# Performance work log

Measured on AMD Instinct MI355X. Metric: run time of the kernel, lower is better.

Reference implementation:

```python
import jax, jax.numpy as jnp
import numpy as np

B, S, D, H, DFF = 2, 2048, 768, 12, 3072
DK = D // H
LN_EPS = 1e-5

def _row_norm(x):
    # L2-normalize along last dim (torch F.normalize semantics)
    n = jnp.sqrt(jnp.sum(x * x, axis=-1, keepdims=True))
    return x / jnp.maximum(n, 1e-12)

def _layer_norm(x, gamma, beta):
    mu = jnp.mean(x, axis=-1, keepdims=True)
    var = jnp.mean((x - mu) ** 2, axis=-1, keepdims=True)
    return (x - mu) * jax.lax.rsqrt(var + LN_EPS) * gamma + beta

def setup_inputs() -> dict:
    key = jax.random.key(0)
    ks = jax.random.split(key, 16)
    sd = 1.0 / np.sqrt(D)
    sf = 1.0 / np.sqrt(DFF)
    inp = {
        "x": jax.random.normal(ks[0], (B, S, D), jnp.float32),
        "Wq": jax.random.uniform(ks[1], (D, D), jnp.float32, -sd, sd),
        "bq": jnp.zeros((D,), jnp.float32),
        "Wk": jax.random.uniform(ks[2], (D, D), jnp.float32, -sd, sd),
        "bk": jnp.zeros((D,), jnp.float32),
        "Wv": jax.random.uniform(ks[3], (D, D), jnp.float32, -sd, sd),
        "bv": jnp.zeros((D,), jnp.float32),
        "Wo": jax.random.uniform(ks[4], (D, D), jnp.float32, -sd, sd),
        "bo": jnp.zeros((D,), jnp.float32),
        "W1": jax.random.uniform(ks[5], (D, DFF), jnp.float32, -sd, sd),
        "b1": jnp.zeros((DFF,), jnp.float32),
        "W2": jax.random.uniform(ks[6], (DFF, D), jnp.float32, -sf, sf),
        "b2": jnp.zeros((D,), jnp.float32),
        "gamma": jnp.ones((D,), jnp.float32),
        "beta": jnp.zeros((D,), jnp.float32),
    }
    return inp

def reference(x, Wq, bq, Wk, bk, Wv, bv, Wo, bo, W1, b1, W2, b2, gamma, beta):
    b, s = x.shape[0], x.shape[1]
    # QKV projections, split into heads: [B,H,S,DK]
    def heads(y):
        return y.reshape(b, s, H, DK).transpose(0, 2, 1, 3)
    Q = heads(x @ Wq + bq)
    K = heads(x @ Wk + bk)
    V = heads(x @ Wv + bv)
    Qn = _row_norm(Q)
    Kn = _row_norm(K)
    scores = jnp.einsum("bhqd,bhkd->bhqk", Qn, Kn)
    attn = scores * scores  # squared dot-product, no softmax
    out = jnp.einsum("bhqk,bhkd->bhqd", attn, V)
    out = out.transpose(0, 2, 1, 3).reshape(b, s, D)
    attn_out = out @ Wo + bo
    x = _layer_norm(x + attn_out, gamma, beta)
    # FFN with exact GELU
    h = jax.nn.gelu(x @ W1 + b1, approximate=False)
    ff = h @ W2 + b2
    x = _layer_norm(x + ff, gamma, beta)  # norm1 reused
    return x
```

## Files before the change

### kernel.cpp

```cpp
#include <hip/hip_runtime.h>
#include <math.h>

using bf16   = __bf16;
using bf16x8 = __attribute__((ext_vector_type(8))) __bf16;
using bf16x4 = __attribute__((ext_vector_type(4))) __bf16;
using f32x4  = __attribute__((ext_vector_type(4))) float;

constexpr int S_   = 2048;
constexpr int D_   = 768;
constexpr int DFF_ = 3072;
constexpr int M_   = 4096;
constexpr int BH_  = 24;

__device__ __forceinline__ f32x4 mfma16(bf16x8 a, bf16x8 b, f32x4 c) {
    return __builtin_amdgcn_mfma_f32_16x16x32_bf16(a, b, c, 0, 0, 0);
}

__device__ __forceinline__ void gload16(const bf16* g, bf16* l) {
    __builtin_amdgcn_global_load_lds(
        (const __attribute__((address_space(1))) void*)g,
        (__attribute__((address_space(3))) void*)l, 16, 0, 0);
}

template<int N> __device__ __forceinline__ void wait_vmcnt() {
    if constexpr (N == 0)      asm volatile("s_waitcnt vmcnt(0)" ::: "memory");
    else if constexpr (N == 4) asm volatile("s_waitcnt vmcnt(4)" ::: "memory");
    else if constexpr (N == 6) asm volatile("s_waitcnt vmcnt(6)" ::: "memory");
    else if constexpr (N == 8) asm volatile("s_waitcnt vmcnt(8)" ::: "memory");
    else static_assert(N == 0, "unsupported vmcnt");
}
__device__ __forceinline__ void wait_lgkm0() {
    asm volatile("s_waitcnt lgkmcnt(0)" ::: "memory");
}

__device__ __forceinline__ int xcd_swz(int orig, int nwg) {
    return (orig & 7) * (nwg >> 3) + (orig >> 3);
}

__device__ __forceinline__ float gelu_f(float v) {
    float y = 1.5957691f * (v + 0.044715f * v * v * v);
    return v / (1.0f + __expf(-y));
}

__global__ __launch_bounds__(256)
void pack_x_kernel(const float* __restrict__ x, bf16* __restrict__ xb) {
    const int i = blockIdx.x * 256 + threadIdx.x;
    float4 v = ((const float4*)x)[i];
    bf16x4 o;
    o[0] = (bf16)v.x; o[1] = (bf16)v.y; o[2] = (bf16)v.z; o[3] = (bf16)v.w;
    ((bf16x4*)xb)[i] = o;
}

__global__ __launch_bounds__(256)
void merge_ao_kernel(const bf16* __restrict__ a, const bf16* __restrict__ b,
                     bf16* __restrict__ o) {
    const long i = ((long)blockIdx.x * 256 + threadIdx.x) * 8;
    bf16x8 va = *(const bf16x8*)&a[i];
    bf16x8 vb = *(const bf16x8*)&b[i];
    bf16x8 vo;
#pragma unroll
    for (int j = 0; j < 8; j++) vo[j] = (bf16)((float)va[j] + (float)vb[j]);
    *(bf16x8*)&o[i] = vo;
}

template<bool FIRST>
__global__ __launch_bounds__(256)
void merge_ln_kernel(const bf16* __restrict__ pp, const float* __restrict__ bias,
                     const float* __restrict__ residf, const bf16* __restrict__ residb,
                     const float* __restrict__ gamma, const float* __restrict__ beta,
                     float* __restrict__ outf, bf16* __restrict__ outb) {
    __shared__ float sa[4], sb[4];
    const int row = blockIdx.x, t = threadIdx.x;
    const bf16* p0 = pp + (long)row * 768;
    const bf16* p1 = pp + (long)M_ * 768 + (long)row * 768;
    float v[3];
#pragma unroll
    for (int i = 0; i < 3; i++) {
        const int c = t + i * 256;
        float y = (float)p0[c] + (float)p1[c] + bias[c];
        if (FIRST) y += residf[(long)row * 768 + c];
        else       y += (float)residb[(long)row * 768 + c];
        v[i] = y;
    }
    float s  = v[0] + v[1] + v[2];
    float ss = v[0] * v[0] + v[1] * v[1] + v[2] * v[2];
#pragma unroll
    for (int o = 32; o; o >>= 1) { s += __shfl_xor(s, o); ss += __shfl_xor(ss, o); }
    if ((t & 63) == 0) { sa[t >> 6] = s; sb[t >> 6] = ss; }
    __syncthreads();
    s  = sa[0] + sa[1] + sa[2] + sa[3];
    ss = sb[0] + sb[1] + sb[2] + sb[3];
    const float mu   = s * (1.0f / 768.0f);
    const float var  = ss * (1.0f / 768.0f) - mu * mu;
    const float rstd = rsqrtf(var + 1e-5f);
#pragma unroll
    for (int i = 0; i < 3; i++) {
        const int c = t + i * 256;
        const float ov = (v[i] - mu) * rstd * gamma[c] + beta[c];
        if (FIRST) outb[(long)row * 768 + c] = (bf16)ov;
        else       outf[(long)row * 768 + c] = ov;
    }
}

__global__ __launch_bounds__(256)
void wt_all_kernel(const float* __restrict__ Wq, const float* __restrict__ Wk,
                   const float* __restrict__ Wv, const float* __restrict__ Wo,
                   const float* __restrict__ W1, const float* __restrict__ W2,
                   bf16* __restrict__ Wqkvt, bf16* __restrict__ Wot,
                   bf16* __restrict__ W1t, bf16* __restrict__ W2t) {
    int bid = blockIdx.x;
    const float* in; bf16* out; int K, N, t;
    if (bid < 576) {
        int m = bid / 144; t = bid % 144; K = 768; N = 768;
        in  = (m == 0) ? Wq : (m == 1) ? Wk : (m == 2) ? Wv : Wo;
        out = (m == 3) ? Wot : Wqkvt + (size_t)m * 768 * 768;
    } else if (bid < 1152) {
        t = bid - 576; K = 768; N = 3072; in = W1; out = W1t;
    } else {
        t = bid - 1152; K = 3072; N = 768; in = W2; out = W2t;
    }
    const int ntx = N / 64;
    const int n0 = (t % ntx) * 64, k0 = (t / ntx) * 64;

    __shared__ __align__(16) bf16 T[64][72];
    const int tt = threadIdx.x;
    const int r  = tt >> 2, c0 = (tt & 3) * 16;
    const float* src = in + (size_t)(k0 + r) * N + n0 + c0;
#pragma unroll
    for (int j = 0; j < 16; j += 4) {
        float4 v = *(const float4*)(src + j);
        T[r][c0 + j + 0] = (bf16)v.x;
        T[r][c0 + j + 1] = (bf16)v.y;
        T[r][c0 + j + 2] = (bf16)v.z;
        T[r][c0 + j + 3] = (bf16)v.w;
    }
    __syncthreads();
    bf16x8 o0, o1;
#pragma unroll
    for (int j = 0; j < 8; j++) { o0[j] = T[c0 + j][r]; o1[j] = T[c0 + 8 + j][r]; }
    bf16* dst = out + (size_t)(n0 + r) * K + k0 + c0;
    *(bf16x8*)(dst)     = o0;
    *(bf16x8*)(dst + 8) = o1;
}

template<int EPI, int K, int BM, int BN, int WR, int WC, int KSPLIT>
__global__ __launch_bounds__(256)
void gemm_bt(const bf16* __restrict__ A, const bf16* __restrict__ Bt,
             const float* __restrict__ bias0, const float* __restrict__ bias1,
             const float* __restrict__ bias2,
             bf16* __restrict__ outb,
             bf16* __restrict__ qo, bf16* __restrict__ ko, bf16* __restrict__ vo) {
    constexpr int MR  = BM / WR / 16;
    constexpr int NR  = BN / WC / 16;
    constexpr int GA  = BM / 32;
    constexpr int GB  = BN / 32;
    constexpr int NPT = GA + GB;
    constexpr int KS  = K / KSPLIT;
    constexpr int NCOL = (EPI == 0) ? 2304 : (EPI == 2) ? 3072 : 768;
    constexpr int NBX  = NCOL / BN;
    __shared__ __align__(16) bf16 Al[2 * BM * 64];
    __shared__ __align__(16) bf16 Bl[2 * BN * 64];
    const int tid  = threadIdx.x;
    const int lane = tid & 63, w = tid >> 6;
    const int wr = w / WC, wc = w % WC;
    const int wg = xcd_swz(blockIdx.x, gridDim.x);
    const int ks = wg % KSPLIT;
    const int tt = wg / KSPLIT;
    const int m0 = (tt / NBX) * BM, n0 = (tt % NBX) * BN;
    const int kb = ks * KS;
    const int g = lane >> 4, q = lane & 15;
    const int srow = lane >> 3;
    const int schunk = (((lane & 7) ^ ((lane >> 3) & 7))) * 8;

    f32x4 acc[MR][NR] = {};

    const bf16* gaA = A  + (long)(m0 + w * (BM / 4) + srow) * K + kb + schunk;
    const bf16* gaB = Bt + (long)(n0 + w * (BN / 4) + srow) * K + kb + schunk;

    auto stage = [&](int buf, int kt) {
#pragma unroll
        for (int i = 0; i < GA; i++)
            gload16(gaA + kt + (long)i * 8 * K,
                    &Al[buf * BM * 64 + (w * (BM / 4) + i * 8) * 64]);
#pragma unroll
        for (int i = 0; i < GB; i++)
            gload16(gaB + kt + (long)i * 8 * K,
                    &Bl[buf * BN * 64 + (w * (BN / 4) + i * 8) * 64]);
    };
    auto compute = [&](int buf) {
#pragma unroll
        for (int c = 0; c < 2; c++) {
            const int rch = ((c * 4 + g) ^ (q & 7)) * 8;
            bf16x8 af[MR], bfr[NR];
#pragma unroll
            for (int i = 0; i < MR; i++)
                af[i] = *(const bf16x8*)
                    &Al[buf * BM * 64 + (wr * (BM / WR) + i * 16 + q) * 64 + rch];
#pragma unroll
            for (int i = 0; i < NR; i++)
                bfr[i] = *(const bf16x8*)
                    &Bl[buf * BN * 64 + (wc * (BN / WC) + i * 16 + q) * 64 + rch];
#pragma unroll
            for (int mi = 0; mi < MR; mi++)
#pragma unroll
                for (int ni = 0; ni < NR; ni++)
                    acc[mi][ni] = mfma16(af[mi], bfr[ni], acc[mi][ni]);
        }
    };

    stage(0, 0);
    stage(1, 64);
    int cur = 0;
    for (int kt = 0; kt < KS - 64; kt += 64) {
        wait_vmcnt<NPT>();
        __builtin_amdgcn_s_barrier();
        compute(cur);
        wait_lgkm0();
        __builtin_amdgcn_s_barrier();
        if (kt + 128 < KS) stage(cur, kt + 128);
        cur ^= 1;
    }
    wait_vmcnt<0>();
    __builtin_amdgcn_s_barrier();
    compute(cur);

#pragma unroll
    for (int mi = 0; mi < MR; mi++) {
        if (EPI == 0) {
            const int col0  = n0 + wc * 64;
            const int which = (col0 >= 1536) ? 2 : (col0 >= 768 ? 1 : 0);
            const int row0  = m0 + wr * (BM / WR) + mi * 16 + g * 4;
            float val[NR][4];
#pragma unroll
            for (int ni = 0; ni < NR; ni++) {
                const int dd = col0 + ni * 16 + q - which * 768;
                const float bias = (which == 0 ? bias0 : which == 1 ? bias1 : bias2)[dd];
#pragma unroll
                for (int r = 0; r < 4; r++) val[ni][r] = acc[mi][ni][r] + bias;
            }
            if (which <= 1) {
#pragma unroll
                for (int r = 0; r < 4; r++) {
                    float ss = val[0][r] * val[0][r];
#pragma unroll
                    for (int ni = 1; ni < NR; ni++) ss += val[ni][r] * val[ni][r];
                    ss += __shfl_xor(ss, 1);
                    ss += __shfl_xor(ss, 2);
                    ss += __shfl_xor(ss, 4);
                    ss += __shfl_xor(ss, 8);
                    const float rn = 1.0f / fmaxf(sqrtf(ss), 1e-12f);
#pragma unroll
                    for (int ni = 0; ni < NR; ni++) val[ni][r] *= rn;
                }
            }
            const int dd0 = col0 - which * 768;
            const int hh  = dd0 >> 6;
            const long bh = (long)(row0 >> 11) * 12 + hh;
#pragma unroll
            for (int ni = 0; ni < NR; ni++) {
                const int dk = ni * 16 + q;
                if (which == 2) {
                    bf16x4 pv;
#pragma unroll
                    for (int r = 0; r < 4; r++) pv[r] = (bf16)val[ni][r];
                    *(bf16x4*)&vo[(bh * 64 + dk) * 2048 + (row0 & 2047)] = pv;
                } else {
                    bf16* dst = (which == 0) ? qo : ko;
#pragma unroll
                    for (int r = 0; r < 4; r++)
                        dst[(bh * 2048 + ((row0 + r) & 2047)) * 64 + dk] = (bf16)val[ni][r];
                }
            }
        } else if (EPI == 2) {
#pragma unroll
            for (int ni = 0; ni < NR; ni++) {
                const int col  = n0 + wc * (BN / WC) + ni * 16 + q;
                const int row0 = m0 + wr * (BM / WR) + mi * 16 + g * 4;
                const float bias = bias0[col];
#pragma unroll
                for (int r = 0; r < 4; r++) {
                    const float v = acc[mi][ni][r] + bias;
                    outb[(long)(row0 + r) * 3072 + col] = (bf16)gelu_f(v);
                }
            }
        } else {
#pragma unroll
            for (int ni = 0; ni < NR; ni++) {
                const int col  = n0 + wc * (BN / WC) + ni * 16 + q;
                const int row0 = m0 + wr * (BM / WR) + mi * 16 + g * 4;
#pragma unroll
                for (int r = 0; r < 4; r++)
                    outb[(long)ks * M_ * 768 + (long)(row0 + r) * 768 + col] =
                        (bf16)acc[mi][ni][r];
            }
        }
    }
}

__global__ __launch_bounds__(256, 3)
void attn_kernel(const bf16* __restrict__ Qn, const bf16* __restrict__ Kn,
                 const bf16* __restrict__ Vt, bf16* __restrict__ AOp) {
    const int wg  = xcd_swz(blockIdx.x, gridDim.x);
    const int bh  = wg >> 5;
    const int rem = wg & 31;
    const int kvhalf = rem >> 4;
    const int qblk   = rem & 15;
    const int tid = threadIdx.x, lane = tid & 63, w = tid >> 6;
    const int g = lane >> 4, q15 = lane & 15;
    const int qbase = qblk * 128 + w * 32;
    const int kv0   = kvhalf * 1024;
    constexpr int NT = 16;

    __shared__ __align__(16) bf16 Kl[2][64][64];
    __shared__ __align__(16) bf16 Vl[2][64][64];
    __shared__ __align__(16) bf16 Pl[4][16][64];
    bf16 (*Pw)[64] = Pl[w];

    const bf16* Qp = Qn + (long)bh * S_ * 64;
    const bf16* Kp = Kn + (long)bh * S_ * 64 + (long)kv0 * 64;
    const bf16* Vp = Vt + (long)bh * 64 * S_ + kv0;
    bf16* AOo = AOp + (long)kvhalf * M_ * D_;

    const int srow = tid >> 3, scol = (tid & 7) * 8;
    const int ssw  = (((lane & 7) ^ ((lane >> 3) & 7))) * 8;
    const int q7   = q15 & 7;

    bf16x8 qf00 = *(const bf16x8*)&Qp[(long)(qbase + q15) * 64 + g * 8];
    bf16x8 qf01 = *(const bf16x8*)&Qp[(long)(qbase + q15) * 64 + 32 + g * 8];
    bf16x8 qf10 = *(const bf16x8*)&Qp[(long)(qbase + 16 + q15) * 64 + g * 8];
    bf16x8 qf11 = *(const bf16x8*)&Qp[(long)(qbase + 16 + q15) * 64 + 32 + g * 8];

    f32x4 o0[4] = {}, o1[4] = {};
    bf16x8 kf[4][2], vf[4][2];
    bf16x8 aK0, aK1, aV0, aV1, bK0, bK1, bV0, bV1;

    auto gloadA = [&](int kt) {
        aK0 = *(const bf16x8*)&Kp[(long)(kt + srow) * 64 + scol];
        aK1 = *(const bf16x8*)&Kp[(long)(kt + 32 + srow) * 64 + scol];
        aV0 = *(const bf16x8*)&Vp[(long)srow * S_ + kt + scol];
        aV1 = *(const bf16x8*)&Vp[(long)(32 + srow) * S_ + kt + scol];
    };
    auto gloadB = [&](int kt) {
        bK0 = *(const bf16x8*)&Kp[(long)(kt + srow) * 64 + scol];
        bK1 = *(const bf16x8*)&Kp[(long)(kt + 32 + srow) * 64 + scol];
        bV0 = *(const bf16x8*)&Vp[(long)srow * S_ + kt + scol];
        bV1 = *(const bf16x8*)&Vp[(long)(32 + srow) * S_ + kt + scol];
    };
    auto stageA = [&](int buf) {
        *(bf16x8*)&Kl[buf][srow][ssw]      = aK0;
        *(bf16x8*)&Kl[buf][32 + srow][ssw] = aK1;
        *(bf16x8*)&Vl[buf][srow][ssw]      = aV0;
        *(bf16x8*)&Vl[buf][32 + srow][ssw] = aV1;
    };
    auto stageB = [&](int buf) {
        *(bf16x8*)&Kl[buf][srow][ssw]      = bK0;
        *(bf16x8*)&Kl[buf][32 + srow][ssw] = bK1;
        *(bf16x8*)&Vl[buf][srow][ssw]      = bV0;
        *(bf16x8*)&Vl[buf][32 + srow][ssw] = bV1;
    };

    auto loadKf = [&](int cur) {
#pragma unroll
        for (int ni = 0; ni < 4; ni++)
#pragma unroll
            for (int c = 0; c < 2; c++)
                kf[ni][c] = *(const bf16x8*)
                    &Kl[cur][ni * 16 + q15][(((c * 4 + g) ^ q7)) * 8];
    };
    auto loadVf = [&](int cur) {
#pragma unroll
        for (int ni = 0; ni < 4; ni++)
#pragma unroll
            for (int c = 0; c < 2; c++)
                vf[ni][c] = *(const bf16x8*)
                    &Vl[cur][ni * 16 + q15][(((c * 4 + g) ^ q7)) * 8];
    };
    auto qk = [&](bf16x8 qa, bf16x8 qb) {
        f32x4 s[4];
#pragma unroll
        for (int ni = 0; ni < 4; ni++) {
            s[ni] = mfma16(kf[ni][0], qa, f32x4{0.f, 0.f, 0.f, 0.f});
            s[ni] = mfma16(kf[ni][1], qb, s[ni]);
        }
#pragma unroll
        for (int ni = 0; ni < 4; ni++) {
            bf16x4 p4;
#pragma unroll
            for (int r = 0; r < 4; r++) { float v = s[ni][r]; p4[r] = (bf16)(v * v); }
            const int ch = (ni * 2 + (g >> 1)) ^ q7;
            *(bf16x4*)&Pw[q15][ch * 8 + (g & 1) * 4] = p4;
        }
    };
    auto pv = [&](f32x4 (&o)[4]) {
        bf16x8 pf0 = *(const bf16x8*)&Pw[q15][((g ^ q7)) * 8];
        bf16x8 pf1 = *(const bf16x8*)&Pw[q15][(((4 + g) ^ q7)) * 8];
#pragma unroll
        for (int ni = 0; ni < 4; ni++) {
            o[ni] = mfma16(pf0, vf[ni][0], o[ni]);
            o[ni] = mfma16(pf1, vf[ni][1], o[ni]);
        }
    };

    gloadA(0);
    stageA(0);
    gloadB(64);
    wait_lgkm0(); __builtin_amdgcn_s_barrier();
    stageB(1);
    gloadA(2 * 64);
    loadKf(0); qk(qf00, qf01);
    loadVf(0); pv(o0);
    qk(qf10, qf11);

    for (int t = 1; t <= NT - 3; t += 2) {
        pv(o1);
        wait_lgkm0(); __builtin_amdgcn_s_barrier();
        stageA(0);
        gloadB((t + 2) * 64);
        loadKf(1); qk(qf00, qf01);
        loadVf(1); pv(o0);
        qk(qf10, qf11);

        pv(o1);
        wait_lgkm0(); __builtin_amdgcn_s_barrier();
        stageB(1);
        if (t + 3 < NT) gloadA((t + 3) * 64);
        loadKf(0); qk(qf00, qf01);
        loadVf(0); pv(o0);
        qk(qf10, qf11);
    }
    pv(o1);
    wait_lgkm0(); __builtin_amdgcn_s_barrier();
    loadKf(1); qk(qf00, qf01);
    loadVf(1); pv(o0);
    qk(qf10, qf11);
    pv(o1);

    const int b = bh / 12, h = bh % 12;
#pragma unroll
    for (int ni = 0; ni < 4; ni++)
#pragma unroll
        for (int r = 0; r < 4; r++) {
            const int s0r = qbase + g * 4 + r;
            AOo[((long)b * S_ + s0r) * D_ + h * 64 + ni * 16 + q15] = (bf16)o0[ni][r];
            const int s1r = qbase + 16 + g * 4 + r;
            AOo[((long)b * S_ + s1r) * D_ + h * 64 + ni * 16 + q15] = (bf16)o1[ni][r];
        }
}

extern "C" void kernel_launch(void* const* d_in, const int* in_sizes, int n_in,
                              void* d_out, int out_size, void* d_ws, size_t ws_size,
                              hipStream_t stream) {
    const float* x     = (const float*)d_in[0];
    const float* Wq    = (const float*)d_in[1];
    const float* bq    = (const float*)d_in[2];
    const float* Wk    = (const float*)d_in[3];
    const float* bk    = (const float*)d_in[4];
    const float* Wv    = (const float*)d_in[5];
    const float* bv    = (const float*)d_in[6];
    const float* Wo    = (const float*)d_in[7];
    const float* bo    = (const float*)d_in[8];
    const float* W1    = (const float*)d_in[9];
    const float* b1    = (const float*)d_in[10];
    const float* W2    = (const float*)d_in[11];
    const float* b2    = (const float*)d_in[12];
    const float* gamma = (const float*)d_in[13];
    const float* beta  = (const float*)d_in[14];

    char* p = (char*)d_ws;
    auto alloc = [&](size_t bytes) -> void* {
        void* r = p;
        p += (bytes + 255) & ~(size_t)255;
        return r;
    };
    bf16*  Xb    = (bf16*)alloc((size_t)M_ * D_ * 2);
    bf16*  Wqkvt = (bf16*)alloc((size_t)2304 * 768 * 2);
    bf16*  Wot   = (bf16*)alloc((size_t)768 * 768 * 2);
    bf16*  W1t   = (bf16*)alloc((size_t)3072 * 768 * 2);
    bf16*  W2t   = (bf16*)alloc((size_t)768 * 3072 * 2);
    bf16*  Qh    = (bf16*)alloc((size_t)BH_ * S_ * 64 * 2);
    bf16*  Kh    = (bf16*)alloc((size_t)BH_ * S_ * 64 * 2);
    bf16*  Vt    = (bf16*)alloc((size_t)BH_ * S_ * 64 * 2);
    bf16*  AOp   = (bf16*)alloc((size_t)2 * M_ * D_ * 2);
    bf16*  AO    = (bf16*)alloc((size_t)M_ * D_ * 2);
    bf16*  pp    = (bf16*)alloc((size_t)2 * M_ * 768 * 2);
    bf16*  x1b   = (bf16*)alloc((size_t)M_ * D_ * 2);
    bf16*  hbuf  = (bf16*)alloc((size_t)M_ * DFF_ * 2);

    pack_x_kernel<<<(M_ * D_) / 1024, 256, 0, stream>>>(x, Xb);
    wt_all_kernel<<<1728, 256, 0, stream>>>(Wq, Wk, Wv, Wo, W1, W2,
                                            Wqkvt, Wot, W1t, W2t);

    gemm_bt<0, 768, 64, 128, 2, 2, 1><<<64 * 18, 256, 0, stream>>>(
        Xb, Wqkvt, bq, bk, bv, nullptr, Qh, Kh, Vt);

    attn_kernel<<<2 * 16 * BH_, 256, 0, stream>>>(Qh, Kh, Vt, AOp);
    merge_ao_kernel<<<(M_ * D_) / 2048, 256, 0, stream>>>(
        AOp, AOp + (size_t)M_ * D_, AO);

    gemm_bt<1, 768, 64, 128, 2, 2, 2><<<64 * 6 * 2, 256, 0, stream>>>(
        AO, Wot, nullptr, nullptr, nullptr, pp, nullptr, nullptr, nullptr);
    merge_ln_kernel<true><<<M_, 256, 0, stream>>>(
        pp, bo, x, nullptr, gamma, beta, nullptr, x1b);

    gemm_bt<2, 768, 64, 128, 2, 2, 1><<<64 * 24, 256, 0, stream>>>(
        x1b, W1t, b1, nullptr, nullptr, hbuf, nullptr, nullptr, nullptr);

    gemm_bt<3, 3072, 64, 128, 2, 2, 2><<<64 * 6 * 2, 256, 0, stream>>>(
        hbuf, W2t, nullptr, nullptr, nullptr, pp, nullptr, nullptr, nullptr);
    merge_ln_kernel<false><<<M_, 256, 0, stream>>>(
        pp, b2, nullptr, x1b, gamma, beta, (float*)d_out, nullptr);
}
```

Measured before the change: 155.9 us.

## Stage K/V tiles via direct global-to-LDS loads with vmcnt-based double buffering

```diff
diff --git a/kernel.cpp b/kernel.cpp
--- a/kernel.cpp
+++ b/kernel.cpp
@@ -321,9 +321,12 @@
     const bf16* Vp = Vt + (long)bh * 64 * S_ + kv0;
     bf16* AOo = AOp + (long)kvhalf * M_ * D_;
 
-    const int srow = tid >> 3, scol = (tid & 7) * 8;
-    const int ssw  = (((lane & 7) ^ ((lane >> 3) & 7))) * 8;
+    const int grow = lane >> 3;
+    const int gch  = (((lane & 7) ^ (lane >> 3))) * 8;
     const int q7   = q15 & 7;
+
+    const bf16* gK = Kp + (long)(w * 16 + grow) * 64 + gch;
+    const bf16* gV = Vp + (long)(w * 16 + grow) * S_ + gch;
 
     bf16x8 qf00 = *(const bf16x8*)&Qp[(long)(qbase + q15) * 64 + g * 8];
     bf16x8 qf01 = *(const bf16x8*)&Qp[(long)(qbase + q15) * 64 + 32 + g * 8];
@@ -332,31 +335,12 @@
 
     f32x4 o0[4] = {}, o1[4] = {};
     bf16x8 kf[4][2], vf[4][2];
-    bf16x8 aK0, aK1, aV0, aV1, bK0, bK1, bV0, bV1;
-
-    auto gloadA = [&](int kt) {
-        aK0 = *(const bf16x8*)&Kp[(long)(kt + srow) * 64 + scol];
-        aK1 = *(const bf16x8*)&Kp[(long)(kt + 32 + srow) * 64 + scol];
-        aV0 = *(const bf16x8*)&Vp[(long)srow * S_ + kt + scol];
-        aV1 = *(const bf16x8*)&Vp[(long)(32 + srow) * S_ + kt + scol];
-    };
-    auto gloadB = [&](int kt) {
-        bK0 = *(const bf16x8*)&Kp[(long)(kt + srow) * 64 + scol];
-        bK1 = *(const bf16x8*)&Kp[(long)(kt + 32 + srow) * 64 + scol];
-        bV0 = *(const bf16x8*)&Vp[(long)srow * S_ + kt + scol];
-        bV1 = *(const bf16x8*)&Vp[(long)(32 + srow) * S_ + kt + scol];
-    };
-    auto stageA = [&](int buf) {
-        *(bf16x8*)&Kl[buf][srow][ssw]      = aK0;
-        *(bf16x8*)&Kl[buf][32 + srow][ssw] = aK1;
-        *(bf16x8*)&Vl[buf][srow][ssw]      = aV0;
-        *(bf16x8*)&Vl[buf][32 + srow][ssw] = aV1;
-    };
-    auto stageB = [&](int buf) {
-        *(bf16x8*)&Kl[buf][srow][ssw]      = bK0;
-        *(bf16x8*)&Kl[buf][32 + srow][ssw] = bK1;
-        *(bf16x8*)&Vl[buf][srow][ssw]      = bV0;
-        *(bf16x8*)&Vl[buf][32 + srow][ssw] = bV1;
+
+    auto stage = [&](int buf, int kt) {
+        gload16(gK + (long)kt * 64,            &Kl[buf][w * 16][0]);
+        gload16(gK + (long)kt * 64 + 8 * 64,   &Kl[buf][w * 16 + 8][0]);
+        gload16(gV + kt,                       &Vl[buf][w * 16][0]);
+        gload16(gV + kt + 8 * S_,              &Vl[buf][w * 16 + 8][0]);
     };
 
     auto loadKf = [&](int cur) {
@@ -400,40 +384,30 @@
             o[ni] = mfma16(pf1, vf[ni][1], o[ni]);
         }
     };
-
-    gloadA(0);
-    stageA(0);
-    gloadB(64);
-    wait_lgkm0(); __builtin_amdgcn_s_barrier();
-    stageB(1);
-    gloadA(2 * 64);
-    loadKf(0); qk(qf00, qf01);
-    loadVf(0); pv(o0);
-    qk(qf10, qf11);
-
-    for (int t = 1; t <= NT - 3; t += 2) {
+    auto compute = [&](int cur) {
+        loadKf(cur);
+        qk(qf00, qf01);
+        loadVf(cur);
+        pv(o0);
+        qk(qf10, qf11);
         pv(o1);
-        wait_lgkm0(); __builtin_amdgcn_s_barrier();
-        stageA(0);
-        gloadB((t + 2) * 64);
-        loadKf(1); qk(qf00, qf01);
-        loadVf(1); pv(o0);
-        qk(qf10, qf11);
-
-        pv(o1);
-        wait_lgkm0(); __builtin_amdgcn_s_barrier();
-        stageB(1);
-        if (t + 3 < NT) gloadA((t + 3) * 64);
-        loadKf(0); qk(qf00, qf01);
-        loadVf(0); pv(o0);
-        qk(qf10, qf11);
-    }
-    pv(o1);
-    wait_lgkm0(); __builtin_amdgcn_s_barrier();
-    loadKf(1); qk(qf00, qf01);
-    loadVf(1); pv(o0);
-    qk(qf10, qf11);
-    pv(o1);
+    };
+
+    stage(0, 0);
+    stage(1, 64);
+    int cur = 0;
+    for (int t = 0; t < NT - 1; t++) {
+        wait_vmcnt<4>();
+        __builtin_amdgcn_s_barrier();
+        compute(cur);
+        wait_lgkm0();
+        __builtin_amdgcn_s_barrier();
+        if (t + 2 < NT) stage(cur, (t + 2) * 64);
+        cur ^= 1;
+    }
+    wait_vmcnt<0>();
+    __builtin_amdgcn_s_barrier();
+    compute(cur);
 
     const int b = bh / 12, h = bh % 12;
 #pragma unroll
```

Measured after the change: 155.1 us. About the same (-0.5%).
